# Performance work log

Hardware: AMD Instinct MI355X
Metric: run time of the kernel (lower is better)

## Reference

```python
import itertools
import jax, jax.numpy as jnp
import numpy as np

NUM_GROUPS = 2  # num_squeeze_group
LN_EPS = 1e-6


def setup_inputs() -> dict:
    key = jax.random.key(0)
    ks = jax.random.split(key, 8)
    B, F, D = 1024, 32, 64
    P = F * (F - 1) // 2  # 496 pairs
    OUT = 512
    g = NUM_GROUPS
    red = max(1, F * g * 2 // 4)  # reduction_ratio = 4 -> 32
    emb_size = F * D
    return {
        "x": jax.random.normal(ks[0], (B, F, D), jnp.float32),
        "W1": jax.random.normal(ks[1], (F * 2 * g, red), jnp.float32) * (1.0 / np.sqrt(F * 2 * g)),
        "b1": jnp.zeros((red,), jnp.float32),
        "W2": jax.random.normal(ks[2], (red, emb_size), jnp.float32) * (1.0 / np.sqrt(red)),
        "b2": jnp.zeros((emb_size,), jnp.float32),
        "ln_scale": jnp.ones((emb_size,), jnp.float32),
        "ln_bias": jnp.zeros((emb_size,), jnp.float32),
        "Wp": jax.random.normal(ks[3], (P, D, D), jnp.float32) * (1.0 / np.sqrt(D)),
        "bp": jnp.zeros((P, D), jnp.float32),
        "Wo": jax.random.normal(ks[4], (P, OUT), jnp.float32) * (1.0 / np.sqrt(P)),
        "bo": jnp.zeros((OUT,), jnp.float32),
    }


def _pair_indices(F):
    pairs = np.array(list(itertools.combinations(range(F), 2)), dtype=np.int32)
    return pairs[:, 0], pairs[:, 1]


def reference(x, W1, b1, W2, b2, ln_scale, ln_bias, Wp, bp, Wo, bo):
    B, F, D = x.shape
    g = NUM_GROUPS

    # ---- SENet ----
    xg = x.reshape(B, F, g, D // g)
    # per-field [max(g), mean(g)], concatenated over fields -> [B, F*2g]
    z = jnp.concatenate([xg.max(axis=-1), xg.mean(axis=-1)], axis=-1).reshape(B, F * 2 * g)
    a1 = jax.nn.relu(z @ W1 + b1)            # [B, red]
    weights = a1 @ W2 + b2                   # [B, F*D]
    flat = x.reshape(B, F * D)
    senet = flat * weights + flat            # skip connection
    # layer norm over last axis
    mu = senet.mean(axis=-1, keepdims=True)
    var = senet.var(axis=-1, keepdims=True)
    senet = (senet - mu) * jax.lax.rsqrt(var + LN_EPS) * ln_scale + ln_bias

    # ---- BiLinear ('interaction', use_plus=True) ----
    i_idx, j_idx = _pair_indices(F)
    xi = x[:, i_idx, :]                      # [B, P, D]
    xj = x[:, j_idx, :]                      # [B, P, D]
    proj = jnp.einsum('bpd,pde->bpe', xi, Wp) + bp  # per-pair Dense(D->D)
    dots = jnp.sum(proj * xj, axis=-1)       # [B, P] batched dot (bi-linear+)
    bilinear = dots @ Wo + bo                # [B, OUT]

    return jnp.concatenate([senet, bilinear], axis=-1)
```

## Files before the change

### kernel.cpp

```cpp
#include <hip/hip_runtime.h>
#include <hip/hip_bf16.h>

#define F_FEAT 32
#define D_DIM 64
#define B_SZ 1024
#define EMB 2048
#define P_PAIRS 496
#define KPAD 512
#define OUT_N 512
#define OUT_STRIDE 2560
#define LN_EPS 1e-6f

typedef __attribute__((ext_vector_type(8))) short bf16x8;
typedef __attribute__((ext_vector_type(4))) float f32x4;

__device__ inline ushort f2bf(float f) {
    union { float f; unsigned u; } a; a.f = f;
    unsigned u = a.u;
    unsigned r = (u + 0x7FFFu + ((u >> 16) & 1u)) >> 16;
    return (ushort)r;
}
__device__ inline float bf2f(ushort u) {
    union { unsigned u; float f; } a; a.u = ((unsigned)u) << 16;
    return a.f;
}

__global__ __launch_bounds__(256) void k_prep(
        const float* __restrict__ Wp, ushort* __restrict__ Wpt,
        const float* __restrict__ Wo, ushort* __restrict__ Wot,
        ushort* __restrict__ db) {
    __shared__ float tile[64][65];
    int t = threadIdx.x;
    int blk = blockIdx.x;

    if (blk < 496) {
        int p = blk;
        const float* src = Wp + (size_t)p * 4096;
        ushort* dst = Wpt + (size_t)p * 4096;
#pragma unroll
        for (int it = 0; it < 4; ++it) {
            int d = it * 16 + (t >> 4);
            int e4 = (t & 15) * 4;
            float4 v = *reinterpret_cast<const float4*>(src + d * 64 + e4);
            tile[d][e4] = v.x; tile[d][e4 + 1] = v.y; tile[d][e4 + 2] = v.z; tile[d][e4 + 3] = v.w;
        }
        __syncthreads();
#pragma unroll
        for (int it = 0; it < 4; ++it) {
            int e = it * 16 + (t >> 4);
            int d4 = (t & 15) * 4;
            ushort4 o;
            o.x = f2bf(tile[d4][e]);     o.y = f2bf(tile[d4 + 1][e]);
            o.z = f2bf(tile[d4 + 2][e]); o.w = f2bf(tile[d4 + 3][e]);
            *reinterpret_cast<ushort4*>(dst + e * 64 + d4) = o;
        }
    } else if (blk < 560) {
        int bidx = blk - 496;
        int k0 = (bidx & 7) * 64;
        int n0 = (bidx >> 3) * 64;
#pragma unroll
        for (int it = 0; it < 4; ++it) {
            int kr = it * 16 + (t >> 4);
            int nc = (t & 15) * 4;
            int k = k0 + kr;
            float4 v = {0.f, 0.f, 0.f, 0.f};
            if (k < P_PAIRS) v = *reinterpret_cast<const float4*>(Wo + (size_t)k * OUT_N + n0 + nc);
            tile[kr][nc] = v.x; tile[kr][nc + 1] = v.y; tile[kr][nc + 2] = v.z; tile[kr][nc + 3] = v.w;
        }
        __syncthreads();
#pragma unroll
        for (int it = 0; it < 4; ++it) {
            int nr = it * 16 + (t >> 4);
            int kc = (t & 15) * 4;
            ushort4 o;
            o.x = f2bf(tile[kc][nr]);     o.y = f2bf(tile[kc + 1][nr]);
            o.z = f2bf(tile[kc + 2][nr]); o.w = f2bf(tile[kc + 3][nr]);
            *reinterpret_cast<ushort4*>(Wot + (size_t)(n0 + nr) * KPAD + k0 + kc) = o;
        }
    } else {
        int tid = (blk - 560) * 256 + t;
        if (tid < B_SZ) {
            bf16x8 z = {0, 0, 0, 0, 0, 0, 0, 0};
            ushort* dstp = db + (size_t)tid * KPAD + P_PAIRS;
            *reinterpret_cast<bf16x8*>(dstp) = z;
            *reinterpret_cast<bf16x8*>(dstp + 8) = z;
        }
    }
}

__global__ __launch_bounds__(512) void k_senet(
        const float* __restrict__ x, ushort* __restrict__ xb,
        const float* __restrict__ W1, const float* __restrict__ b1,
        const float* __restrict__ W2, const float* __restrict__ b2,
        const float* __restrict__ ln_s, const float* __restrict__ ln_b,
        float* __restrict__ out) {
    __shared__ float xs[4][EMB];
    __shared__ float zs[4][128];
    __shared__ float a1s[4][32];
    __shared__ float red[2][4][8];
    int t = threadIdx.x;
    int b0 = blockIdx.x * 4;

    for (int r = 0; r < 4; ++r) {
        const float4* src = reinterpret_cast<const float4*>(x + (size_t)(b0 + r) * EMB);
        float4 v = src[t];
        reinterpret_cast<float4*>(&xs[r][0])[t] = v;
        ushort4 o;
        o.x = f2bf(v.x); o.y = f2bf(v.y); o.z = f2bf(v.z); o.w = f2bf(v.w);
        *reinterpret_cast<ushort4*>(xb + (size_t)(b0 + r) * EMB + t * 4) = o;
    }
    __syncthreads();

    if (t < 256) {
        int r = t >> 6, f = (t >> 1) & 31, gg = t & 1;
        const float* base = &xs[r][f * 64 + gg * 32];
        float mx = -INFINITY, sm = 0.f;
        for (int q = 0; q < 32; ++q) {
            float v = base[(q + t) & 31];
            mx = fmaxf(mx, v); sm += v;
        }
        zs[r][f * 4 + gg]     = mx;
        zs[r][f * 4 + 2 + gg] = sm * (1.f / 32.f);
    }
    __syncthreads();

    if (t < 128) {
        int r = t >> 5, c = t & 31;
        float acc = b1[c];
        for (int k = 0; k < 128; ++k) acc += zs[r][k] * W1[k * 32 + c];
        a1s[r][c] = fmaxf(acc, 0.f);
    }
    __syncthreads();

    float acc[4][4];
#pragma unroll
    for (int r = 0; r < 4; ++r)
#pragma unroll
        for (int u = 0; u < 4; ++u) acc[r][u] = 0.f;

    for (int k = 0; k < 32; ++k) {
        float a0 = a1s[0][k], a1v = a1s[1][k], a2 = a1s[2][k], a3 = a1s[3][k];
#pragma unroll
        for (int u = 0; u < 4; ++u) {
            float wv = W2[k * EMB + t + 512 * u];
            acc[0][u] += a0 * wv; acc[1][u] += a1v * wv;
            acc[2][u] += a2 * wv; acc[3][u] += a3 * wv;
        }
    }
    float ssum[4], ssq[4];
#pragma unroll
    for (int r = 0; r < 4; ++r) { ssum[r] = 0.f; ssq[r] = 0.f; }
#pragma unroll
    for (int r = 0; r < 4; ++r) {
#pragma unroll
        for (int u = 0; u < 4; ++u) {
            int e = t + 512 * u;
            float w = acc[r][u] + b2[e];
            float s = xs[r][e] * (w + 1.0f);
            xs[r][e] = s;
            ssum[r] += s; ssq[r] += s * s;
        }
    }
    int lane = t & 63, w = t >> 6;
#pragma unroll
    for (int r = 0; r < 4; ++r) {
        float a = ssum[r], q = ssq[r];
        for (int off = 32; off; off >>= 1) { a += __shfl_down(a, off); q += __shfl_down(q, off); }
        if (lane == 0) { red[0][r][w] = a; red[1][r][w] = q; }
    }
    __syncthreads();
    float mu[4], rs[4];
#pragma unroll
    for (int r = 0; r < 4; ++r) {
        float a = 0.f, q = 0.f;
#pragma unroll
        for (int i = 0; i < 8; ++i) { a += red[0][r][i]; q += red[1][r][i]; }
        mu[r] = a * (1.f / 2048.f);
        float var = q * (1.f / 2048.f) - mu[r] * mu[r];
        rs[r] = rsqrtf(var + LN_EPS);
    }
#pragma unroll
    for (int r = 0; r < 4; ++r) {
#pragma unroll
        for (int u = 0; u < 4; ++u) {
            int e = t + 512 * u;
            float s = xs[r][e];
            out[(size_t)(b0 + r) * OUT_STRIDE + e] = (s - mu[r]) * rs[r] * ln_s[e] + ln_b[e];
        }
    }
}

__global__ __launch_bounds__(256) void k_dots(
        const ushort* __restrict__ xb, const ushort* __restrict__ Wpt,
        const float* __restrict__ bp, ushort* __restrict__ db) {
    int p = blockIdx.x >> 1;
    int h = blockIdx.x & 1;
    int i = 0, rem = p;
    while (rem >= F_FEAT - 1 - i) { rem -= F_FEAT - 1 - i; ++i; }
    int j = i + 1 + rem;

    int wave = threadIdx.x >> 6, lane = threadIdx.x & 63;
    int row = lane & 15, kg = lane >> 4;

    bf16x8 wfr[4][2];
#pragma unroll
    for (int nt = 0; nt < 4; ++nt)
#pragma unroll
        for (int ks = 0; ks < 2; ++ks)
            wfr[nt][ks] = *reinterpret_cast<const bf16x8*>(
                Wpt + (size_t)p * 4096 + (nt * 16 + row) * 64 + ks * 32 + kg * 8);

    f32x4 bb[4];
#pragma unroll
    for (int nt = 0; nt < 4; ++nt)
        bb[nt] = *reinterpret_cast<const f32x4*>(bp + p * 64 + nt * 16 + kg * 4);

#pragma unroll
    for (int it = 0; it < 8; ++it) {
        int b0 = h * 512 + (wave * 8 + it) * 16;

        bf16x8 xifr[2];
#pragma unroll
        for (int ks = 0; ks < 2; ++ks)
            xifr[ks] = *reinterpret_cast<const bf16x8*>(
                xb + (size_t)(b0 + row) * EMB + i * 64 + ks * 32 + kg * 8);

        ushort4 xjw[4];
#pragma unroll
        for (int nt = 0; nt < 4; ++nt)
            xjw[nt] = *reinterpret_cast<const ushort4*>(
                xb + (size_t)(b0 + row) * EMB + j * 64 + nt * 16 + kg * 4);

        f32x4 acc[4];
#pragma unroll
        for (int nt = 0; nt < 4; ++nt) {
            f32x4 z = {0.f, 0.f, 0.f, 0.f};
            acc[nt] = z;
            acc[nt] = __builtin_amdgcn_mfma_f32_16x16x32_bf16(wfr[nt][0], xifr[0], acc[nt], 0, 0, 0);
            acc[nt] = __builtin_amdgcn_mfma_f32_16x16x32_bf16(wfr[nt][1], xifr[1], acc[nt], 0, 0, 0);
        }

        float v = 0.f;
#pragma unroll
        for (int nt = 0; nt < 4; ++nt) {
            v += (acc[nt][0] + bb[nt][0]) * bf2f(xjw[nt].x);
            v += (acc[nt][1] + bb[nt][1]) * bf2f(xjw[nt].y);
            v += (acc[nt][2] + bb[nt][2]) * bf2f(xjw[nt].z);
            v += (acc[nt][3] + bb[nt][3]) * bf2f(xjw[nt].w);
        }
        v += __shfl_xor(v, 16);
        v += __shfl_xor(v, 32);
        if (lane < 16)
            db[(size_t)(b0 + lane) * KPAD + p] = f2bf(v);
    }
}

__global__ __launch_bounds__(256) void k_bilin2(
        const ushort* __restrict__ db, const ushort* __restrict__ Wot,
        const float* __restrict__ bo, float* __restrict__ out) {
    int mt  = blockIdx.x >> 4;
    int nt0 = blockIdx.x & 15;
    int wave = threadIdx.x >> 6, lane = threadIdx.x & 63;
    int row = lane & 15, kg = lane >> 4;
    int m0 = mt * 64 + wave * 16;
    int n0 = nt0 * 32;

    f32x4 acc0 = {0.f, 0.f, 0.f, 0.f};
    f32x4 acc1 = {0.f, 0.f, 0.f, 0.f};
    const ushort* arow  = db  + (size_t)(m0 + row) * KPAD + kg * 8;
    const ushort* brow0 = Wot + (size_t)(n0 + row) * KPAD + kg * 8;
    const ushort* brow1 = brow0 + 16 * KPAD;
#pragma unroll
    for (int ks = 0; ks < 16; ++ks) {
        bf16x8 a  = *reinterpret_cast<const bf16x8*>(arow  + ks * 32);
        bf16x8 b0 = *reinterpret_cast<const bf16x8*>(brow0 + ks * 32);
        bf16x8 b1 = *reinterpret_cast<const bf16x8*>(brow1 + ks * 32);
        acc0 = __builtin_amdgcn_mfma_f32_16x16x32_bf16(a, b0, acc0, 0, 0, 0);
        acc1 = __builtin_amdgcn_mfma_f32_16x16x32_bf16(a, b1, acc1, 0, 0, 0);
    }
    int col = row;
    float bo0 = bo[n0 + col], bo1 = bo[n0 + 16 + col];
#pragma unroll
    for (int r = 0; r < 4; ++r) {
        size_t orow = (size_t)(m0 + kg * 4 + r) * OUT_STRIDE + 2048 + n0;
        out[orow + col]      = acc0[r] + bo0;
        out[orow + 16 + col] = acc1[r] + bo1;
    }
}

extern "C" void kernel_launch(void* const* d_in, const int* in_sizes, int n_in,
                              void* d_out, int out_size, void* d_ws, size_t ws_size,
                              hipStream_t stream) {
    const float* x    = (const float*)d_in[0];
    const float* W1   = (const float*)d_in[1];
    const float* b1   = (const float*)d_in[2];
    const float* W2   = (const float*)d_in[3];
    const float* b2   = (const float*)d_in[4];
    const float* ln_s = (const float*)d_in[5];
    const float* ln_b = (const float*)d_in[6];
    const float* Wp   = (const float*)d_in[7];
    const float* bp   = (const float*)d_in[8];
    const float* Wo   = (const float*)d_in[9];
    const float* bo   = (const float*)d_in[10];
    float* out = (float*)d_out;

    ushort* xb   = (ushort*)d_ws;
    ushort* wpt  = (ushort*)((char*)d_ws + 4194304);
    ushort* db   = (ushort*)((char*)d_ws + 4194304 + 4063232);
    ushort* wot  = (ushort*)((char*)d_ws + 4194304 + 4063232 + 1048576);

    k_prep<<<568, 256, 0, stream>>>(Wp, wpt, Wo, wot, db);
    k_senet<<<B_SZ / 4, 512, 0, stream>>>(x, xb, W1, b1, W2, b2, ln_s, ln_b, out);
    k_dots<<<P_PAIRS * 2, 256, 0, stream>>>(xb, wpt, bp, db);
    k_bilin2<<<256, 256, 0, stream>>>(db, wot, bo, out);
}
```

Before: 59.18 us.

## Merge SENet into bilinear tail kernel and move x bf16 cast into prep

Cuts the launch sequence from four kernels to three. The fp32-to-bf16 conversion of x moves into the prep kernel, which now runs 512-thread blocks. The SENet/LayerNorm work and the final bilinear GEMM share one launch, with separate block ranges (256 SENet blocks plus 128 GEMM blocks with 64x64 tiles), so independent work overlaps instead of running serially. The per-pair bias is also folded into the MFMA accumulator initialisation, which removes adds from the epilogue. The SENet blocks use about 35 KB of LDS and share a launch with the GEMM blocks, which may limit co-residency.

```diff
diff --git a/kernel.cpp b/kernel.cpp
--- a/kernel.cpp
+++ b/kernel.cpp
@@ -25,7 +25,8 @@
     return a.f;
 }
 
-__global__ __launch_bounds__(256) void k_prep(
+__global__ __launch_bounds__(512) void k_prep(
+        const float* __restrict__ x, ushort* __restrict__ xb,
         const float* __restrict__ Wp, ushort* __restrict__ Wpt,
         const float* __restrict__ Wo, ushort* __restrict__ Wot,
         ushort* __restrict__ db) {
@@ -33,34 +34,42 @@
     int t = threadIdx.x;
     int blk = blockIdx.x;
 
-    if (blk < 496) {
-        int p = blk;
+    if (blk < 512) {
+        size_t base = ((size_t)blk * 512 + t) * 8;
+        float4 v0 = *reinterpret_cast<const float4*>(x + base);
+        float4 v1 = *reinterpret_cast<const float4*>(x + base + 4);
+        bf16x8 o;
+        o[0] = f2bf(v0.x); o[1] = f2bf(v0.y); o[2] = f2bf(v0.z); o[3] = f2bf(v0.w);
+        o[4] = f2bf(v1.x); o[5] = f2bf(v1.y); o[6] = f2bf(v1.z); o[7] = f2bf(v1.w);
+        *reinterpret_cast<bf16x8*>(xb + base) = o;
+    } else if (blk < 1008) {
+        int p = blk - 512;
         const float* src = Wp + (size_t)p * 4096;
         ushort* dst = Wpt + (size_t)p * 4096;
 #pragma unroll
-        for (int it = 0; it < 4; ++it) {
-            int d = it * 16 + (t >> 4);
+        for (int it = 0; it < 2; ++it) {
+            int d = it * 32 + (t >> 4);
             int e4 = (t & 15) * 4;
             float4 v = *reinterpret_cast<const float4*>(src + d * 64 + e4);
             tile[d][e4] = v.x; tile[d][e4 + 1] = v.y; tile[d][e4 + 2] = v.z; tile[d][e4 + 3] = v.w;
         }
         __syncthreads();
 #pragma unroll
-        for (int it = 0; it < 4; ++it) {
-            int e = it * 16 + (t >> 4);
+        for (int it = 0; it < 2; ++it) {
+            int e = it * 32 + (t >> 4);
             int d4 = (t & 15) * 4;
             ushort4 o;
             o.x = f2bf(tile[d4][e]);     o.y = f2bf(tile[d4 + 1][e]);
             o.z = f2bf(tile[d4 + 2][e]); o.w = f2bf(tile[d4 + 3][e]);
             *reinterpret_cast<ushort4*>(dst + e * 64 + d4) = o;
         }
-    } else if (blk < 560) {
-        int bidx = blk - 496;
+    } else if (blk < 1072) {
+        int bidx = blk - 1008;
         int k0 = (bidx & 7) * 64;
         int n0 = (bidx >> 3) * 64;
 #pragma unroll
-        for (int it = 0; it < 4; ++it) {
-            int kr = it * 16 + (t >> 4);
+        for (int it = 0; it < 2; ++it) {
+            int kr = it * 32 + (t >> 4);
             int nc = (t & 15) * 4;
             int k = k0 + kr;
             float4 v = {0.f, 0.f, 0.f, 0.f};
@@ -69,8 +78,8 @@
         }
         __syncthreads();
 #pragma unroll
-        for (int it = 0; it < 4; ++it) {
-            int nr = it * 16 + (t >> 4);
+        for (int it = 0; it < 2; ++it) {
+            int nr = it * 32 + (t >> 4);
             int kc = (t & 15) * 4;
             ushort4 o;
             o.x = f2bf(tile[kc][nr]);     o.y = f2bf(tile[kc + 1][nr]);
@@ -78,114 +87,12 @@
             *reinterpret_cast<ushort4*>(Wot + (size_t)(n0 + nr) * KPAD + k0 + kc) = o;
         }
     } else {
-        int tid = (blk - 560) * 256 + t;
+        int tid = (blk - 1072) * 512 + t;
         if (tid < B_SZ) {
             bf16x8 z = {0, 0, 0, 0, 0, 0, 0, 0};
             ushort* dstp = db + (size_t)tid * KPAD + P_PAIRS;
             *reinterpret_cast<bf16x8*>(dstp) = z;
             *reinterpret_cast<bf16x8*>(dstp + 8) = z;
-        }
-    }
-}
-
-__global__ __launch_bounds__(512) void k_senet(
-        const float* __restrict__ x, ushort* __restrict__ xb,
-        const float* __restrict__ W1, const float* __restrict__ b1,
-        const float* __restrict__ W2, const float* __restrict__ b2,
-        const float* __restrict__ ln_s, const float* __restrict__ ln_b,
-        float* __restrict__ out) {
-    __shared__ float xs[4][EMB];
-    __shared__ float zs[4][128];
-    __shared__ float a1s[4][32];
-    __shared__ float red[2][4][8];
-    int t = threadIdx.x;
-    int b0 = blockIdx.x * 4;
-
-    for (int r = 0; r < 4; ++r) {
-        const float4* src = reinterpret_cast<const float4*>(x + (size_t)(b0 + r) * EMB);
-        float4 v = src[t];
-        reinterpret_cast<float4*>(&xs[r][0])[t] = v;
-        ushort4 o;
-        o.x = f2bf(v.x); o.y = f2bf(v.y); o.z = f2bf(v.z); o.w = f2bf(v.w);
-        *reinterpret_cast<ushort4*>(xb + (size_t)(b0 + r) * EMB + t * 4) = o;
-    }
-    __syncthreads();
-
-    if (t < 256) {
-        int r = t >> 6, f = (t >> 1) & 31, gg = t & 1;
-        const float* base = &xs[r][f * 64 + gg * 32];
-        float mx = -INFINITY, sm = 0.f;
-        for (int q = 0; q < 32; ++q) {
-            float v = base[(q + t) & 31];
-            mx = fmaxf(mx, v); sm += v;
-        }
-        zs[r][f * 4 + gg]     = mx;
-        zs[r][f * 4 + 2 + gg] = sm * (1.f / 32.f);
-    }
-    __syncthreads();
-
-    if (t < 128) {
-        int r = t >> 5, c = t & 31;
-        float acc = b1[c];
-        for (int k = 0; k < 128; ++k) acc += zs[r][k] * W1[k * 32 + c];
-        a1s[r][c] = fmaxf(acc, 0.f);
-    }
-    __syncthreads();
-
-    float acc[4][4];
-#pragma unroll
-    for (int r = 0; r < 4; ++r)
-#pragma unroll
-        for (int u = 0; u < 4; ++u) acc[r][u] = 0.f;
-
-    for (int k = 0; k < 32; ++k) {
-        float a0 = a1s[0][k], a1v = a1s[1][k], a2 = a1s[2][k], a3 = a1s[3][k];
-#pragma unroll
-        for (int u = 0; u < 4; ++u) {
-            float wv = W2[k * EMB + t + 512 * u];
-            acc[0][u] += a0 * wv; acc[1][u] += a1v * wv;
-            acc[2][u] += a2 * wv; acc[3][u] += a3 * wv;
-        }
-    }
-    float ssum[4], ssq[4];
-#pragma unroll
-    for (int r = 0; r < 4; ++r) { ssum[r] = 0.f; ssq[r] = 0.f; }
-#pragma unroll
-    for (int r = 0; r < 4; ++r) {
-#pragma unroll
-        for (int u = 0; u < 4; ++u) {
-            int e = t + 512 * u;
-            float w = acc[r][u] + b2[e];
-            float s = xs[r][e] * (w + 1.0f);
-            xs[r][e] = s;
-            ssum[r] += s; ssq[r] += s * s;
-        }
-    }
-    int lane = t & 63, w = t >> 6;
-#pragma unroll
-    for (int r = 0; r < 4; ++r) {
-        float a = ssum[r], q = ssq[r];
-        for (int off = 32; off; off >>= 1) { a += __shfl_down(a, off); q += __shfl_down(q, off); }
-        if (lane == 0) { red[0][r][w] = a; red[1][r][w] = q; }
-    }
-    __syncthreads();
-    float mu[4], rs[4];
-#pragma unroll
-    for (int r = 0; r < 4; ++r) {
-        float a = 0.f, q = 0.f;
-#pragma unroll
-        for (int i = 0; i < 8; ++i) { a += red[0][r][i]; q += red[1][r][i]; }
-        mu[r] = a * (1.f / 2048.f);
-        float var = q * (1.f / 2048.f) - mu[r] * mu[r];
-        rs[r] = rsqrtf(var + LN_EPS);
-    }
-#pragma unroll
-    for (int r = 0; r < 4; ++r) {
-#pragma unroll
-        for (int u = 0; u < 4; ++u) {
-            int e = t + 512 * u;
-            float s = xs[r][e];
-            out[(size_t)(b0 + r) * OUT_STRIDE + e] = (s - mu[r]) * rs[r] * ln_s[e] + ln_b[e];
         }
     }
 }
@@ -234,8 +141,7 @@
         f32x4 acc[4];
 #pragma unroll
         for (int nt = 0; nt < 4; ++nt) {
-            f32x4 z = {0.f, 0.f, 0.f, 0.f};
-            acc[nt] = z;
+            acc[nt] = bb[nt];
             acc[nt] = __builtin_amdgcn_mfma_f32_16x16x32_bf16(wfr[nt][0], xifr[0], acc[nt], 0, 0, 0);
             acc[nt] = __builtin_amdgcn_mfma_f32_16x16x32_bf16(wfr[nt][1], xifr[1], acc[nt], 0, 0, 0);
         }
@@ -243,10 +149,10 @@
         float v = 0.f;
 #pragma unroll
         for (int nt = 0; nt < 4; ++nt) {
-            v += (acc[nt][0] + bb[nt][0]) * bf2f(xjw[nt].x);
-            v += (acc[nt][1] + bb[nt][1]) * bf2f(xjw[nt].y);
-            v += (acc[nt][2] + bb[nt][2]) * bf2f(xjw[nt].z);
-            v += (acc[nt][3] + bb[nt][3]) * bf2f(xjw[nt].w);
+            v += acc[nt][0] * bf2f(xjw[nt].x);
+            v += acc[nt][1] * bf2f(xjw[nt].y);
+            v += acc[nt][2] * bf2f(xjw[nt].z);
+            v += acc[nt][3] * bf2f(xjw[nt].w);
         }
         v += __shfl_xor(v, 16);
         v += __shfl_xor(v, 32);
@@ -255,36 +161,136 @@
     }
 }
 
-__global__ __launch_bounds__(256) void k_bilin2(
+__global__ __launch_bounds__(512) void k_tail(
+        const float* __restrict__ x,
+        const float* __restrict__ W1, const float* __restrict__ b1,
+        const float* __restrict__ W2, const float* __restrict__ b2,
+        const float* __restrict__ ln_s, const float* __restrict__ ln_b,
         const ushort* __restrict__ db, const ushort* __restrict__ Wot,
         const float* __restrict__ bo, float* __restrict__ out) {
-    int mt  = blockIdx.x >> 4;
-    int nt0 = blockIdx.x & 15;
-    int wave = threadIdx.x >> 6, lane = threadIdx.x & 63;
-    int row = lane & 15, kg = lane >> 4;
-    int m0 = mt * 64 + wave * 16;
-    int n0 = nt0 * 32;
-
-    f32x4 acc0 = {0.f, 0.f, 0.f, 0.f};
-    f32x4 acc1 = {0.f, 0.f, 0.f, 0.f};
-    const ushort* arow  = db  + (size_t)(m0 + row) * KPAD + kg * 8;
-    const ushort* brow0 = Wot + (size_t)(n0 + row) * KPAD + kg * 8;
-    const ushort* brow1 = brow0 + 16 * KPAD;
-#pragma unroll
-    for (int ks = 0; ks < 16; ++ks) {
-        bf16x8 a  = *reinterpret_cast<const bf16x8*>(arow  + ks * 32);
-        bf16x8 b0 = *reinterpret_cast<const bf16x8*>(brow0 + ks * 32);
-        bf16x8 b1 = *reinterpret_cast<const bf16x8*>(brow1 + ks * 32);
-        acc0 = __builtin_amdgcn_mfma_f32_16x16x32_bf16(a, b0, acc0, 0, 0, 0);
-        acc1 = __builtin_amdgcn_mfma_f32_16x16x32_bf16(a, b1, acc1, 0, 0, 0);
-    }
-    int col = row;
-    float bo0 = bo[n0 + col], bo1 = bo[n0 + 16 + col];
-#pragma unroll
-    for (int r = 0; r < 4; ++r) {
-        size_t orow = (size_t)(m0 + kg * 4 + r) * OUT_STRIDE + 2048 + n0;
-        out[orow + col]      = acc0[r] + bo0;
-        out[orow + 16 + col] = acc1[r] + bo1;
+    __shared__ float xs[4][EMB];
+    __shared__ float zs[4][128];
+    __shared__ float a1s[4][32];
+    __shared__ float red[2][4][8];
+    int t = threadIdx.x;
+
+    if (blockIdx.x >= 256) {
+        int bid = blockIdx.x - 256;
+        int mt  = bid >> 3;
+        int nt0 = bid & 7;
+        int wave = t >> 6, lane = t & 63;
+        int row = lane & 15, kg = lane >> 4;
+        int m0 = mt * 64 + (wave >> 1) * 16;
+        int n0 = nt0 * 64 + (wave & 1) * 32;
+
+        f32x4 acc0 = {0.f, 0.f, 0.f, 0.f};
+        f32x4 acc1 = {0.f, 0.f, 0.f, 0.f};
+        const ushort* arow  = db  + (size_t)(m0 + row) * KPAD + kg * 8;
+        const ushort* brow0 = Wot + (size_t)(n0 + row) * KPAD + kg * 8;
+        const ushort* brow1 = brow0 + 16 * KPAD;
+#pragma unroll
+        for (int ks = 0; ks < 16; ++ks) {
+            bf16x8 a  = *reinterpret_cast<const bf16x8*>(arow  + ks * 32);
+            bf16x8 b0 = *reinterpret_cast<const bf16x8*>(brow0 + ks * 32);
+            bf16x8 b1 = *reinterpret_cast<const bf16x8*>(brow1 + ks * 32);
+            acc0 = __builtin_amdgcn_mfma_f32_16x16x32_bf16(a, b0, acc0, 0, 0, 0);
+            acc1 = __builtin_amdgcn_mfma_f32_16x16x32_bf16(a, b1, acc1, 0, 0, 0);
+        }
+        int col = row;
+        float bo0 = bo[n0 + col], bo1 = bo[n0 + 16 + col];
+#pragma unroll
+        for (int r = 0; r < 4; ++r) {
+            size_t orow = (size_t)(m0 + kg * 4 + r) * OUT_STRIDE + 2048 + n0;
+            out[orow + col]      = acc0[r] + bo0;
+            out[orow + 16 + col] = acc1[r] + bo1;
+        }
+        return;
+    }
+
+    int b0 = blockIdx.x * 4;
+
+    for (int r = 0; r < 4; ++r) {
+        const float4* src = reinterpret_cast<const float4*>(x + (size_t)(b0 + r) * EMB);
+        reinterpret_cast<float4*>(&xs[r][0])[t] = src[t];
+    }
+    __syncthreads();
+
+    if (t < 256) {
+        int r = t >> 6, f = (t >> 1) & 31, gg = t & 1;
+        const float* base = &xs[r][f * 64 + gg * 32];
+        float mx = -INFINITY, sm = 0.f;
+        for (int q = 0; q < 32; ++q) {
+            float v = base[(q + t) & 31];
+            mx = fmaxf(mx, v); sm += v;
+        }
+        zs[r][f * 4 + gg]     = mx;
+        zs[r][f * 4 + 2 + gg] = sm * (1.f / 32.f);
+    }
+    __syncthreads();
+
+    if (t < 128) {
+        int r = t >> 5, c = t & 31;
+        float acc = b1[c];
+        for (int k = 0; k < 128; ++k) acc += zs[r][k] * W1[k * 32 + c];
+        a1s[r][c] = fmaxf(acc, 0.f);
+    }
+    __syncthreads();
+
+    float acc[4][4];
+#pragma unroll
+    for (int r = 0; r < 4; ++r)
+#pragma unroll
+        for (int u = 0; u < 4; ++u) acc[r][u] = 0.f;
+
+    for (int k = 0; k < 32; ++k) {
+        float a0 = a1s[0][k], a1v = a1s[1][k], a2 = a1s[2][k], a3 = a1s[3][k];
+#pragma unroll
+        for (int u = 0; u < 4; ++u) {
+            float wv = W2[k * EMB + t + 512 * u];
+            acc[0][u] += a0 * wv; acc[1][u] += a1v * wv;
+            acc[2][u] += a2 * wv; acc[3][u] += a3 * wv;
+        }
+    }
+    float ssum[4], ssq[4];
+#pragma unroll
+    for (int r = 0; r < 4; ++r) { ssum[r] = 0.f; ssq[r] = 0.f; }
+#pragma unroll
+    for (int r = 0; r < 4; ++r) {
+#pragma unroll
+        for (int u = 0; u < 4; ++u) {
+            int e = t + 512 * u;
+            float w = acc[r][u] + b2[e];
+            float s = xs[r][e] * (w + 1.0f);
+            xs[r][e] = s;
+            ssum[r] += s; ssq[r] += s * s;
+        }
+    }
+    int lane = t & 63, w = t >> 6;
+#pragma unroll
+    for (int r = 0; r < 4; ++r) {
+        float a = ssum[r], q = ssq[r];
+        for (int off = 32; off; off >>= 1) { a += __shfl_down(a, off); q += __shfl_down(q, off); }
+        if (lane == 0) { red[0][r][w] = a; red[1][r][w] = q; }
+    }
+    __syncthreads();
+    float mu[4], rs[4];
+#pragma unroll
+    for (int r = 0; r < 4; ++r) {
+        float a = 0.f, q = 0.f;
+#pragma unroll
+        for (int i = 0; i < 8; ++i) { a += red[0][r][i]; q += red[1][r][i]; }
+        mu[r] = a * (1.f / 2048.f);
+        float var = q * (1.f / 2048.f) - mu[r] * mu[r];
+        rs[r] = rsqrtf(var + LN_EPS);
+    }
+#pragma unroll
+    for (int r = 0; r < 4; ++r) {
+#pragma unroll
+        for (int u = 0; u < 4; ++u) {
+            int e = t + 512 * u;
+            float s = xs[r][e];
+            out[(size_t)(b0 + r) * OUT_STRIDE + e] = (s - mu[r]) * rs[r] * ln_s[e] + ln_b[e];
+        }
     }
 }
 
@@ -309,8 +315,7 @@
     ushort* db   = (ushort*)((char*)d_ws + 4194304 + 4063232);
     ushort* wot  = (ushort*)((char*)d_ws + 4194304 + 4063232 + 1048576);
 
-    k_prep<<<568, 256, 0, stream>>>(Wp, wpt, Wo, wot, db);
-    k_senet<<<B_SZ / 4, 512, 0, stream>>>(x, xb, W1, b1, W2, b2, ln_s, ln_b, out);
+    k_prep<<<1074, 512, 0, stream>>>(x, xb, Wp, wpt, Wo, wot, db);
     k_dots<<<P_PAIRS * 2, 256, 0, stream>>>(xb, wpt, bp, db);
-    k_bilin2<<<256, 256, 0, stream>>>(db, wot, bo, out);
-}
+    k_tail<<<384, 512, 0, stream>>>(x, W1, b1, W2, b2, ln_s, ln_b, db, wot, bo, out);
+}
```

Measured after the change: 59.15 us. No clear change (-0.0%).
